# Kernel optimization log

Hardware: AMD Instinct MI355X
Metric: run time of the kernel (lower is better)

## Reference

```python
import jax, jax.numpy as jnp
import numpy as np

N_U = 20000; N_I = 20000; D = 256
NNZ = 600000; EGG = 300000; EDD = 300000; B = 8192
DROP = 0.1; LAM2 = 1e-7


def _attention(x, W, a, edges):
    # GAT-style attention over sampled relationship edges (src -> tgt).
    n, d = x.shape
    h = x @ W                                  # [n, d]
    src, tgt = edges[0], edges[1]
    e = jax.nn.leaky_relu((h @ a[:d])[src] + (h @ a[d:])[tgt], 0.2)  # [E]
    m = jax.ops.segment_max(e, tgt, num_segments=n)
    m = jnp.where(jnp.isfinite(m), m, 0.0)
    ex = jnp.exp(e - m[tgt])
    denom = jax.ops.segment_sum(ex, tgt, num_segments=n)             # [n]
    num = jax.ops.segment_sum(ex[:, None] * h[src], tgt, num_segments=n)  # [n, d]
    return num / (denom[:, None] + 1e-9)


def _spmm(rows, cols, vals, x, n_out):
    # sparse [n_out, n_in] @ dense [n_in, d]
    return jax.ops.segment_sum(vals[:, None] * x[cols], rows, num_segments=n_out)


def _mlp(x, W1, b1, W2, b2, W3, b3):
    h = jax.nn.relu(x @ W1 + b1)
    h = jax.nn.relu(h @ W2 + b2)
    return (h @ W3 + b3)[..., 0]


def setup_inputs() -> dict:
    key = jax.random.key(0)
    ks = jax.random.split(key, 24)
    s = 0.02
    inp = {
        'E_g_0': jax.random.normal(ks[0], (N_U, D), jnp.float32) * s,
        'E_d_0': jax.random.normal(ks[1], (N_I, D), jnp.float32) * s,
        'att_W': jax.random.normal(ks[2], (D, D), jnp.float32) * s,
        'att_a': jax.random.normal(ks[3], (2 * D,), jnp.float32) * s,
        'att1_W': jax.random.normal(ks[4], (D, D), jnp.float32) * s,
        'att1_a': jax.random.normal(ks[5], (2 * D,), jnp.float32) * s,
        'W1': jax.random.normal(ks[6], (2 * D, D), jnp.float32) * s,
        'b1': jnp.zeros((D,), jnp.float32),
        'W2': jax.random.normal(ks[7], (D, D), jnp.float32) * s,
        'b2': jnp.zeros((D,), jnp.float32),
        'W3': jax.random.normal(ks[8], (D, 1), jnp.float32) * s,
        'b3': jnp.zeros((1,), jnp.float32),
        'M1': jax.random.normal(ks[9], (2 * D, D), jnp.float32) * s,
        'mb1': jnp.zeros((D,), jnp.float32),
        'M2': jax.random.normal(ks[10], (D, D), jnp.float32) * s,
        'mb2': jnp.zeros((D,), jnp.float32),
        'adj_vals': jax.random.uniform(ks[11], (NNZ,), jnp.float32),
        'uids': jax.random.randint(ks[12], (B,), 0, N_U, jnp.int32),
        'iids': jax.random.randint(ks[13], (B,), 0, N_I, jnp.int32),
        'pos': jax.random.randint(ks[14], (B,), 0, N_I, jnp.int32),
        'neg': jax.random.randint(ks[15], (B,), 0, N_I, jnp.int32),
        'gene_edges': jax.random.randint(ks[16], (2, EGG), 0, N_U, jnp.int32),
        'drug_edges': jax.random.randint(ks[17], (2, EDD), 0, N_I, jnp.int32),
        'adj_rows': jax.random.randint(ks[18], (NNZ,), 0, N_U, jnp.int32),
        'adj_cols': jax.random.randint(ks[19], (NNZ,), 0, N_I, jnp.int32),
        'drop1': jax.random.bernoulli(ks[20], 1.0 - DROP, (NNZ,)),
        'drop2': jax.random.bernoulli(ks[21], 1.0 - DROP, (NNZ,)),
    }
    return inp


def reference(E_g_0, E_d_0, att_W, att_a, att1_W, att1_a, W1, b1, W2, b2, W3, b3,
              M1, mb1, M2, mb2, adj_vals, uids, iids, pos, neg,
              gene_edges, drug_edges, adj_rows, adj_cols, drop1, drop2):
    # Attention-modulated layer-0 embeddings
    E_d0 = 0.1 * _attention(E_d_0, att_W, att_a, drug_edges) + E_d_0
    E_g0 = 0.1 * _attention(E_g_0, att_W, att_a, gene_edges) + E_g_0

    # sparse_dropout + spmm (two independent dropout draws, as in the source)
    scale = 1.0 / (1.0 - DROP)
    v1 = adj_vals * drop1.astype(adj_vals.dtype) * scale
    v2 = adj_vals * drop2.astype(adj_vals.dtype) * scale
    E_g = _spmm(adj_rows, adj_cols, v1, E_d0, N_U)   # adj @ E_d0
    E_d = _spmm(adj_cols, adj_rows, v2, E_g0, N_I)   # adj.T @ E_g0

    u = E_g[uids]; p = E_d[pos]; ng = E_d[neg]
    pos_s = _mlp(jnp.concatenate([u, p], axis=-1), W1, b1, W2, b2, W3, b3)
    neg_s = _mlp(jnp.concatenate([u, ng], axis=-1), W1, b1, W2, b2, W3, b3)

    # BCE-with-logits (labels 1 for pos, 0 for neg) + BPR term
    loss_pos = jnp.mean(jax.nn.softplus(-pos_s))
    loss_neg = jnp.mean(jax.nn.softplus(neg_s))
    loss_bpr = jnp.mean(jax.nn.softplus(-(pos_s - neg_s)))
    loss_r = loss_pos + loss_neg + loss_bpr

    params = (E_g_0, E_d_0, att_W, att_a, att1_W, att1_a,
              W1, b1, W2, b2, W3, b3, M1, mb1, M2, mb2)
    loss_reg = LAM2 * sum(jnp.sum(p_ * p_) for p_ in params)

    loss = loss_reg + loss_r  # loss_s == 0
    return jnp.stack([loss, loss_r, jnp.zeros((), loss.dtype)])
```

## Files before the change

### kernel.cpp

```cpp
#include <hip/hip_runtime.h>
#include <math.h>

#define N_NODES 20000
#define D       256
#define NNZ     600000
#define NEDGE   300000
#define BATCH   8192
#define DROP_SCALE (1.0f/0.9f)
#define LAM2_F  1e-7f

#define M_PAD   20096
#define CSTRIDE 20032

#define C_ATT 56
#define C_ADJ 80

#define BINW 320
#define NBIN 63
#define TILE_E 2048
#define EPT 8
#define T_ATT ((NEDGE + TILE_E - 1) / TILE_E)
#define T_ADJ ((NNZ + TILE_E - 1) / TILE_E)
#define NBLK_P1 (2 * T_ATT + 2 * T_ADJ)
#define CAP_BIN_ATT 5376
#define CAP_BIN_ADJ 9216

#define FP8_SCALE 256.0f
#define VSCALE    58980.0f
#define INV_VSCALE (1.0f/58980.0f)

typedef unsigned short u16;
typedef unsigned char  u8;
typedef __attribute__((ext_vector_type(8))) short bf16x8;
typedef __attribute__((ext_vector_type(4))) float f32x4;
typedef __attribute__((ext_vector_type(2))) float f32x2;
typedef __attribute__((ext_vector_type(4))) unsigned v4u;

__device__ inline float wave_reduce(float v) {
    #pragma unroll
    for (int off = 32; off > 0; off >>= 1) v += __shfl_down(v, off, 64);
    return v;
}

__device__ inline float softplus_f(float x) {
    float r = log1pf(__expf(-fabsf(x)));
    return x > 0.f ? x + r : r;
}

__device__ inline u16 f2bf(float f) {
    unsigned u = __float_as_uint(f);
    unsigned r = u + 0x7fff + ((u >> 16) & 1);
    return (u16)(r >> 16);
}
__device__ inline float bf2f(u16 b) { return __uint_as_float(((unsigned)b) << 16); }

__device__ inline u16 f2h(float f) {
    _Float16 h = (_Float16)f;
    return __builtin_bit_cast(u16, h);
}
__device__ inline float h2f(u16 b) {
    return (float)__builtin_bit_cast(_Float16, b);
}

__device__ inline unsigned f32x4_to_fp8x4(float a, float b, float c, float d) {
    int r = 0;
    r = __builtin_amdgcn_cvt_pk_fp8_f32(a, b, r, false);
    r = __builtin_amdgcn_cvt_pk_fp8_f32(c, d, r, true);
    return (unsigned)r;
}
__device__ inline u8 f32_to_fp8(float a) {
    int r = __builtin_amdgcn_cvt_pk_fp8_f32(a, a, 0, false);
    return (u8)(r & 0xff);
}

__device__ inline void gld_lds16(const void* g, void* l) {
    __builtin_amdgcn_global_load_lds((const __attribute__((address_space(1))) void*)g,
                                     (__attribute__((address_space(3))) void*)l, 16, 0, 0);
}

struct RegArgs { const float* p[14]; int n[14]; };

__device__ inline void gemm_tile_k(const u16* __restrict__ A, const u16* __restrict__ BT, int K,
                                   int bm, int bn, short (*As)[32], short (*Bs)[32],
                                   f32x4 (&acr)[4][4]) {
    int tid = threadIdx.x, wave = tid >> 6, lane = tid & 63;
    int sr = lane >> 2, sc = (lane & 3) * 8;
    int wr = (wave >> 1) * 64, wc = (wave & 1) * 64;
    int fr = lane & 15, fk = (lane >> 4) * 8;
    for (int k0 = 0; k0 < K; k0 += 32) {
        #pragma unroll
        for (int j = 0; j < 2; j++) {
            int r0 = wave * 32 + j * 16;
            gld_lds16(A  + (size_t)(bm + r0 + sr) * K + k0 + sc, &As[r0][0]);
            gld_lds16(BT + (size_t)(bn + r0 + sr) * K + k0 + sc, &Bs[r0][0]);
        }
        __syncthreads();
        bf16x8 af[4], bfr[4];
        #pragma unroll
        for (int i = 0; i < 4; i++) af[i]  = *(const bf16x8*)&As[wr + i*16 + fr][fk];
        #pragma unroll
        for (int j = 0; j < 4; j++) bfr[j] = *(const bf16x8*)&Bs[wc + j*16 + fr][fk];
        #pragma unroll
        for (int i = 0; i < 4; i++)
            #pragma unroll
            for (int j = 0; j < 4; j++)
                acr[i][j] = __builtin_amdgcn_mfma_f32_16x16x32_bf16(af[i], bfr[j], acr[i][j], 0, 0, 0);
        __syncthreads();
    }
}

__global__ __launch_bounds__(1024) void init_kernel(const float* __restrict__ att_W,
                                                    const float* __restrict__ att_a,
                                                    float* __restrict__ wlv, float* __restrict__ wrv,
                                                    int* __restrict__ zbase, int zwords) {
    int tid = threadIdx.x;
    for (int i = tid; i < zwords; i += 1024) zbase[i] = 0;
    int t = tid & 255, q = tid >> 8;
    float s1 = 0.f, s2 = 0.f;
    for (int n = q * 64; n < q * 64 + 64; n++) {
        float w = att_W[(size_t)t * D + n];
        s1 += w * att_a[n];
        s2 += w * att_a[D + n];
    }
    __shared__ float r1[4][256], r2[4][256];
    r1[q][t] = s1; r2[q][t] = s2;
    __syncthreads();
    if (q == 0) {
        wlv[t] = r1[0][t] + r1[1][t] + r1[2][t] + r1[3][t];
        wrv[t] = r2[0][t] + r2[1][t] + r2[2][t] + r2[3][t];
    }
}

#define NB_CAST (2 * M_PAD / 4)
#define NB_T1   (D * D / 256)
#define NB_T2   (2 * D * D / 256)
#define NB_T3   (D * D / 256)
#define NB_PREP (NB_CAST + NB_T1 + NB_T2 + NB_T3)
#define NB_REG  448
__global__ __launch_bounds__(256) void p1prep_kernel(
        const int* __restrict__ dtgt, const int* __restrict__ dsrc,
        const int* __restrict__ gtgt, const int* __restrict__ gsrc,
        const int* __restrict__ ar,   const int* __restrict__ ac,
        const float* __restrict__ vals,
        const void* __restrict__ drop1, const void* __restrict__ drop2,
        int* __restrict__ pcur, unsigned* __restrict__ attbin, uint2* __restrict__ adjbin,
        const float* __restrict__ E_g, const float* __restrict__ E_d,
        u16* __restrict__ Eg_bf, u16* __restrict__ Ed_bf,
        const float* __restrict__ att_W,
        const float* __restrict__ W1, const float* __restrict__ W2,
        u16* __restrict__ attWT, u16* __restrict__ W1T, u16* __restrict__ W2T,
        const float* __restrict__ wlv, const float* __restrict__ wrv,
        float* __restrict__ hl_g, float* __restrict__ hr_g,
        float* __restrict__ hl_d, float* __restrict__ hr_d,
        float* __restrict__ regp, RegArgs ra, float* __restrict__ acc) {
    if (blockIdx.x < NBLK_P1) {
        __shared__ int hist[NBIN];
        __shared__ int basep[NBIN];
        for (int i = threadIdx.x; i < NBIN; i += 256) hist[i] = 0;
        __syncthreads();

        int b = blockIdx.x;
        int s, t0;
        if (b < T_ATT)               { s = 0; t0 = b; }
        else if (b < 2 * T_ATT)      { s = 1; t0 = b - T_ATT; }
        else if (b < 2*T_ATT + T_ADJ){ s = 2; t0 = b - 2 * T_ATT; }
        else                         { s = 3; t0 = b - 2 * T_ATT - T_ADJ; }
        int base = t0 * TILE_E;
        int regN = (s < 2) ? NEDGE : NNZ;

        int bins[EPT], rank[EPT];
        unsigned key[EPT], pay[EPT];
        float pv[EPT];

        if (s < 2) {
            const int* tgt = (s == 0) ? dtgt : gtgt;
            const int* src = (s == 0) ? dsrc : gsrc;
            #pragma unroll
            for (int e = 0; e < EPT; e++) {
                int idx = base + e * 256 + threadIdx.x;
                rank[e] = -1;
                if (idx < regN) {
                    int k = __builtin_nontemporal_load(tgt + idx);
                    int sv = __builtin_nontemporal_load(src + idx);
                    key[e] = (unsigned)k; pay[e] = (unsigned)sv;
                    bins[e] = k / BINW;
                    rank[e] = atomicAdd(&hist[bins[e]], 1);
                }
            }
        } else {
            const int* keyp = (s == 2) ? ar : ac;
            const int* othp = (s == 2) ? ac : ar;
            const void* drp = (s == 2) ? drop1 : drop2;
            bool nzs = ((const u8*)drp)[4 * threadIdx.x + 1] != 0;
            const bool bf = __popcll(__ballot(nzs)) > 16;
            #pragma unroll
            for (int e = 0; e < EPT; e++) {
                int idx = base + e * 256 + threadIdx.x;
                rank[e] = -1;
                if (idx < regN) {
                    bool keep = bf ? (__builtin_nontemporal_load((const u8*)drp + idx) != 0)
                                   : (__builtin_nontemporal_load((const unsigned*)drp + idx) != 0);
                    if (keep) {
                        int k = __builtin_nontemporal_load(keyp + idx);
                        float v = __builtin_nontemporal_load(vals + idx) * DROP_SCALE;
                        int oth = __builtin_nontemporal_load(othp + idx);
                        key[e] = (unsigned)k; pay[e] = (unsigned)oth; pv[e] = v;
                        bins[e] = k / BINW;
                        rank[e] = atomicAdd(&hist[bins[e]], 1);
                    }
                }
            }
        }
        __syncthreads();
        for (int i = threadIdx.x; i < NBIN; i += 256) {
            int h = hist[i];
            basep[i] = h ? atomicAdd(&pcur[s * NBIN + i], h) : 0;
        }
        __syncthreads();
        if (s < 2) {
            unsigned* seg = attbin + (size_t)s * NBIN * CAP_BIN_ATT;
            #pragma unroll
            for (int e = 0; e < EPT; e++) {
                if (rank[e] < 0) continue;
                int pos = basep[bins[e]] + rank[e];
                if (pos < CAP_BIN_ATT)
                    seg[(size_t)bins[e] * CAP_BIN_ATT + pos] = key[e] | (pay[e] << 16);
            }
        } else {
            uint2* seg = adjbin + (size_t)(s - 2) * NBIN * CAP_BIN_ADJ;
            #pragma unroll
            for (int e = 0; e < EPT; e++) {
                if (rank[e] < 0) continue;
                int pos = basep[bins[e]] + rank[e];
                if (pos < CAP_BIN_ADJ) {
                    uint2 pr; pr.x = key[e] | (pay[e] << 16); pr.y = __float_as_uint(pv[e]);
                    seg[(size_t)bins[e] * CAP_BIN_ADJ + pos] = pr;
                }
            }
        }
    } else {
        int bid = blockIdx.x - NBLK_P1;
        int w = threadIdx.x >> 6, lane = threadIdx.x & 63;
        if (bid < NB_CAST) {
            int wid  = (bid * 256 + threadIdx.x) >> 6;
            int is_d = (wid >= M_PAD);
            int row  = is_d ? wid - M_PAD : wid;
            u16* dst = (is_d ? Ed_bf : Eg_bf) + (size_t)row * D;
            float s3 = 0.f;
            if (row >= N_NODES) {
                ((ushort4*)dst)[lane] = make_ushort4(0, 0, 0, 0);
            } else {
                const float* src = (is_d ? E_d : E_g) + (size_t)row * D;
                float4 e  = ((const float4*)src)[lane];
                float4 l4 = ((const float4*)wlv)[lane];
                float4 r4 = ((const float4*)wrv)[lane];
                ((ushort4*)dst)[lane] = make_ushort4(f2bf(e.x), f2bf(e.y), f2bf(e.z), f2bf(e.w));
                float s1 = e.x*l4.x + e.y*l4.y + e.z*l4.z + e.w*l4.w;
                float s2 = e.x*r4.x + e.y*r4.y + e.z*r4.z + e.w*r4.w;
                s3 = e.x*e.x + e.y*e.y + e.z*e.z + e.w*e.w;
                s1 = wave_reduce(s1); s2 = wave_reduce(s2);
                if (lane == 0) {
                    if (is_d) { hl_d[row] = s1; hr_d[row] = s2; }
                    else      { hl_g[row] = s1; hr_g[row] = s2; }
                }
            }
            s3 = wave_reduce(s3);
            __shared__ float sm3[4];
            if (lane == 0) sm3[threadIdx.x >> 6] = s3;
            __syncthreads();
            if (threadIdx.x == 0) regp[bid] = sm3[0] + sm3[1] + sm3[2] + sm3[3];
        } else if (bid < NB_CAST + NB_T1) {
            int o = (bid - NB_CAST) * 256 + threadIdx.x;
            int n = o >> 8, k = o & 255;
            attWT[o] = f2bf(att_W[(size_t)k * D + n]);
        } else if (bid < NB_CAST + NB_T1 + NB_T2) {
            int o = (bid - NB_CAST - NB_T1) * 256 + threadIdx.x;
            int n = o / (2 * D), k = o - n * (2 * D);
            W1T[o] = f2bf(W1[(size_t)k * D + n]);
        } else if (bid < NB_PREP) {
            int o = (bid - NB_CAST - NB_T1 - NB_T2) * 256 + threadIdx.x;
            int n = o >> 8, k = o & 255;
            W2T[o] = f2bf(W2[(size_t)k * D + n]);
        } else {
            int rb = bid - NB_PREP;
            const float* p = ra.p[rb >> 5];
            int n = ra.n[rb >> 5];
            int base = (rb & 31) * 4096;
            if (base >= n) return;
            float sum = 0.f;
            if (base + 4096 <= n) {
                const float4* p4 = (const float4*)(p + base);
                float4 v = p4[threadIdx.x];
                sum += v.x*v.x + v.y*v.y + v.z*v.z + v.w*v.w;
                v = p4[256 + threadIdx.x];
                sum += v.x*v.x + v.y*v.y + v.z*v.z + v.w*v.w;
                v = p4[512 + threadIdx.x];
                sum += v.x*v.x + v.y*v.y + v.z*v.z + v.w*v.w;
                v = p4[768 + threadIdx.x];
                sum += v.x*v.x + v.y*v.y + v.z*v.z + v.w*v.w;
            } else {
                for (int i = base + threadIdx.x; i < n; i += 256) { float v = p[i]; sum += v * v; }
            }
            sum = wave_reduce(sum);
            __shared__ float smr[4];
            if (lane == 0) smr[w] = sum;
            __syncthreads();
            if (threadIdx.x == 0)
                atomicAdd(&acc[0], smr[0] + smr[1] + smr[2] + smr[3]);
        }
    }
}

#define NB_P2   (4 * NBIN)
#define NB_ATTG ((M_PAD / 128) * 4)
__global__ __launch_bounds__(256) void p2gemm_kernel(
        const int* __restrict__ pcur, const unsigned* __restrict__ attbin,
        const uint2* __restrict__ adjbin,
        const float* __restrict__ hl_d, const float* __restrict__ hr_d,
        const float* __restrict__ hl_g, const float* __restrict__ hr_g,
        int* __restrict__ cnt, unsigned* __restrict__ srcs, unsigned* __restrict__ adj,
        const u16* __restrict__ Eg_bf, const u16* __restrict__ Ed_bf,
        const u16* __restrict__ attWT, u8* __restrict__ h_g, u8* __restrict__ h_d) {
    if (blockIdx.x < NB_P2) {
        int s   = blockIdx.x / NBIN;
        int bin = blockIdx.x - s * NBIN;
        int nodeBase = bin * BINW;
        __shared__ int cur[BINW];
        for (int t = threadIdx.x; t < BINW; t += 256) cur[t] = 0;
        __syncthreads();
        if (s < 2) {
            int m = pcur[s * NBIN + bin]; if (m > CAP_BIN_ATT) m = CAP_BIN_ATT;
            const unsigned* seg = attbin + ((size_t)s * NBIN + bin) * CAP_BIN_ATT;
            const float* hl = (s == 0) ? hl_d : hl_g;
            const float* hr = (s == 0) ? hr_d : hr_g;
            for (int k = threadIdx.x; k < m; k += 256) {
                unsigned e = seg[k];
                int lk  = (int)(e & 0xFFFFu) - nodeBase;
                int src = (int)(e >> 16);
                float ev = hl[src] + hr[nodeBase + lk];
                ev = ev > 0.f ? ev : 0.2f * ev;
                u16 xh = f2h(__expf(ev));
                int c = atomicAdd(&cur[lk], 1);
                if (c < C_ATT)
                    srcs[(size_t)s * N_NODES * C_ATT + (size_t)(nodeBase + lk) * C_ATT + c] =
                        (unsigned)src | ((unsigned)xh << 16);
            }
            __syncthreads();
            for (int t = threadIdx.x; t < BINW; t += 256) {
                int node = nodeBase + t;
                if (node < N_NODES) {
                    int n = cur[t]; if (n > C_ATT) n = C_ATT;
                    cnt[s * CSTRIDE + node] = n;
                }
            }
        } else {
            int m = pcur[s * NBIN + bin]; if (m > CAP_BIN_ADJ) m = CAP_BIN_ADJ;
            const uint2* seg = adjbin + ((size_t)(s - 2) * NBIN + bin) * CAP_BIN_ADJ;
            for (int k = threadIdx.x; k < m; k += 256) {
                uint2 e = seg[k];
                int lk  = (int)(e.x & 0xFFFFu) - nodeBase;
                int oth = (int)(e.x >> 16);
                float v = __uint_as_float(e.y);
                unsigned pk = ((unsigned)(v * VSCALE + 0.5f) << 16) | (unsigned)oth;
                int c = atomicAdd(&cur[lk], 1);
                if (c < C_ADJ)
                    adj[(size_t)(s - 2) * N_NODES * C_ADJ + (size_t)(nodeBase + lk) * C_ADJ + c] = pk;
            }
            __syncthreads();
            for (int t = threadIdx.x; t < BINW; t += 256) {
                int node = nodeBase + t;
                if (node < N_NODES) {
                    int n = cur[t]; if (n > C_ADJ) n = C_ADJ;
                    cnt[s * CSTRIDE + node] = n;
                }
            }
        }
    } else {
        int t  = blockIdx.x - NB_P2;
        int z  = t / (2 * (M_PAD / 128));
        int r  = t - z * (2 * (M_PAD / 128));
        int by = r / (M_PAD / 128);
        int bx = r - by * (M_PAD / 128);
        const u16* A = z ? Ed_bf : Eg_bf;
        u8* C = z ? h_d : h_g;
        __shared__ __align__(16) short As[128][32];
        __shared__ __align__(16) short Bs[128][32];
        int wave = threadIdx.x >> 6, lane = threadIdx.x & 63;
        int bm = bx * 128, bn = by * 128;
        f32x4 acr[4][4];
        #pragma unroll
        for (int i = 0; i < 4; i++)
            #pragma unroll
            for (int j = 0; j < 4; j++)
                #pragma unroll
                for (int q = 0; q < 4; q++) acr[i][j][q] = 0.f;
        gemm_tile_k(A, attWT, D, bm, bn, As, Bs, acr);
        int wr = (wave >> 1) * 64, wc = (wave & 1) * 64, fr = lane & 15;
        #pragma unroll
        for (int j = 0; j < 4; j++) {
            int col = bn + wc + j * 16 + fr;
            #pragma unroll
            for (int i = 0; i < 4; i++) {
                #pragma unroll
                for (int q = 0; q < 4; q++) {
                    int row = bm + wr + i * 16 + (lane >> 4) * 4 + q;
                    if (row < N_NODES)
                        C[(size_t)row * D + col] = f32_to_fp8(acr[i][j][q] * FP8_SCALE);
                }
            }
        }
    }
}

__global__ __launch_bounds__(256) void gemm_bf16(const u16* __restrict__ A, const u16* __restrict__ BT,
                                                 void* __restrict__ C, int M, int N, int K,
                                                 const float* __restrict__ bias, int do_relu, int out_mode,
                                                 const float* __restrict__ w3) {
    __shared__ __align__(16) short As[128][32];
    __shared__ __align__(16) short Bs[128][32];
    int tid = threadIdx.x;
    int wave = tid >> 6, lane = tid & 63;
    int bm = blockIdx.x * 128, bn = blockIdx.y * 128;

    f32x4 acr[4][4];
    #pragma unroll
    for (int i = 0; i < 4; i++)
        #pragma unroll
        for (int j = 0; j < 4; j++)
            #pragma unroll
            for (int r = 0; r < 4; r++) acr[i][j][r] = 0.f;

    gemm_tile_k(A, BT, K, bm, bn, As, Bs, acr);

    int wr = (wave >> 1) * 64, wc = (wave & 1) * 64, fr = lane & 15;

    if (out_mode == 2) {
        __shared__ float sacc[128];
        for (int t = tid; t < 128; t += 256) sacc[t] = 0.f;
        __syncthreads();
        float bvj[4], w3j[4];
        #pragma unroll
        for (int j = 0; j < 4; j++) {
            int col = bn + wc + j * 16 + fr;
            bvj[j] = bias[col];
            w3j[j] = w3[col];
        }
        #pragma unroll
        for (int i = 0; i < 4; i++) {
            #pragma unroll
            for (int r = 0; r < 4; r++) {
                float rs = 0.f;
                #pragma unroll
                for (int j = 0; j < 4; j++) {
                    float v = fmaxf(acr[i][j][r] + bvj[j], 0.f);
                    rs += v * w3j[j];
                }
                rs += __shfl_xor(rs, 1, 64);
                rs += __shfl_xor(rs, 2, 64);
                rs += __shfl_xor(rs, 4, 64);
                rs += __shfl_xor(rs, 8, 64);
                if (fr == 0)
                    atomicAdd(&sacc[wr + i * 16 + (lane >> 4) * 4 + r], rs);
            }
        }
        __syncthreads();
        float* sb = (float*)C;
        for (int t = tid; t < 128; t += 256)
            atomicAdd(&sb[bm + t], sacc[t]);
        return;
    }

    #pragma unroll
    for (int j = 0; j < 4; j++) {
        int col = bn + wc + j * 16 + fr;
        float bv = bias ? bias[col] : 0.f;
        #pragma unroll
        for (int i = 0; i < 4; i++) {
            #pragma unroll
            for (int r = 0; r < 4; r++) {
                int row = bm + wr + i * 16 + (lane >> 4) * 4 + r;
                if (row < M) {
                    float v = acr[i][j][r] + bv;
                    if (do_relu) v = fmaxf(v, 0.f);
                    ((u16*)C)[(size_t)row * N + col] = f2bf(v);
                }
            }
        }
    }
}

__global__ __launch_bounds__(256) void att_kernel(const u8* __restrict__ h_d, const u8* __restrict__ h_g,
                                                  const int* __restrict__ cur, const unsigned* __restrict__ srcs,
                                                  const u16* __restrict__ Ed_bf, const u16* __restrict__ Eg_bf,
                                                  u8* __restrict__ E_d0p, u8* __restrict__ E_g0p) {
    int wid  = (blockIdx.x * blockDim.x + threadIdx.x) >> 6;
    int lane = threadIdx.x & 63;
    if (wid >= 2 * N_NODES) return;
    int is_g = (wid >= N_NODES);
    int node = is_g ? wid - N_NODES : wid;
    const unsigned* h32 = (const unsigned*)(is_g ? h_g : h_d);
    int reg = is_g ? 1 : 0;
    const unsigned* sv = srcs + (size_t)reg * N_NODES * C_ATT + (size_t)node * C_ATT;
    int n = cur[reg * CSTRIDE + node];
    if (n > C_ATT) n = C_ATT;
    float ax = 0.f, ay = 0.f, az = 0.f, aw = 0.f, denom = 0.f;
    int k = 0;
    for (; k + 8 <= n; k += 8) {
        v4u qa = __builtin_nontemporal_load((const v4u*)(sv + k));
        v4u qb = __builtin_nontemporal_load((const v4u*)(sv + k + 4));
        unsigned g[8]; float x[8];
        #pragma unroll
        for (int j = 0; j < 4; j++) {
            g[j]     = h32[((size_t)(qa[j] & 0xFFFFu) << 6) + lane];
            g[4 + j] = h32[((size_t)(qb[j] & 0xFFFFu) << 6) + lane];
            x[j]     = h2f((u16)(qa[j] >> 16));
            x[4 + j] = h2f((u16)(qb[j] >> 16));
        }
        #pragma unroll
        for (int j = 0; j < 8; j++) {
            denom += x[j];
            f32x2 lo = __builtin_amdgcn_cvt_pk_f32_fp8(g[j], false);
            f32x2 hi = __builtin_amdgcn_cvt_pk_f32_fp8(g[j], true);
            ax += x[j]*lo[0]; ay += x[j]*lo[1]; az += x[j]*hi[0]; aw += x[j]*hi[1];
        }
    }
    for (; k + 4 <= n; k += 4) {
        v4u qa = __builtin_nontemporal_load((const v4u*)(sv + k));
        unsigned g[4]; float x[4];
        #pragma unroll
        for (int j = 0; j < 4; j++) {
            g[j] = h32[((size_t)(qa[j] & 0xFFFFu) << 6) + lane];
            x[j] = h2f((u16)(qa[j] >> 16));
        }
        #pragma unroll
        for (int j = 0; j < 4; j++) {
            denom += x[j];
            f32x2 lo = __builtin_amdgcn_cvt_pk_f32_fp8(g[j], false);
            f32x2 hi = __builtin_amdgcn_cvt_pk_f32_fp8(g[j], true);
            ax += x[j]*lo[0]; ay += x[j]*lo[1]; az += x[j]*hi[0]; aw += x[j]*hi[1];
        }
    }
    for (; k < n; k++) {
        unsigned q = sv[k];
        float xv = h2f((u16)(q >> 16));
        unsigned g = h32[((size_t)(q & 0xFFFFu) << 6) + lane];
        denom += xv;
        f32x2 lo = __builtin_amdgcn_cvt_pk_f32_fp8(g, false);
        f32x2 hi = __builtin_amdgcn_cvt_pk_f32_fp8(g, true);
        ax += xv*lo[0]; ay += xv*lo[1]; az += xv*hi[0]; aw += xv*hi[1];
    }
    float sc = 0.1f / (denom + 1e-9f);
    const u16* E0b = is_g ? Eg_bf : Ed_bf;
    u8*       out  = is_g ? E_g0p : E_d0p;
    ushort4 b4 = ((const ushort4*)(E0b + (size_t)node * D))[lane];
    unsigned pk = f32x4_to_fp8x4(FP8_SCALE * bf2f(b4.x) + sc * ax, FP8_SCALE * bf2f(b4.y) + sc * ay,
                                 FP8_SCALE * bf2f(b4.z) + sc * az, FP8_SCALE * bf2f(b4.w) + sc * aw);
    ((unsigned*)(out + (size_t)node * D))[lane] = pk;
}

__global__ __launch_bounds__(256) void pull_kernel(const int* __restrict__ uids, const int* __restrict__ pos,
                                                   const int* __restrict__ neg,
                                                   const int* __restrict__ cur, const unsigned* __restrict__ adj,
                                                   const u8* __restrict__ E_d0p, const u8* __restrict__ E_g0p,
                                                   u16* __restrict__ X) {
    int wid  = (blockIdx.x * blockDim.x + threadIdx.x) >> 6;
    int lane = threadIdx.x & 63;
    if (wid >= 3 * BATCH) return;
    int type = wid >> 13;
    int b    = wid & (BATCH - 1);
    int node, reg; const u8* E;
    if (type == 0)      { node = uids[b]; reg = 2; E = E_d0p; }
    else if (type == 1) { node = pos[b];  reg = 3; E = E_g0p; }
    else                { node = neg[b];  reg = 3; E = E_g0p; }
    const unsigned* E32 = (const unsigned*)E;
    const unsigned* av = adj + (size_t)(reg - 2) * N_NODES * C_ADJ + (size_t)node * C_ADJ;
    int n = cur[reg * CSTRIDE + node];
    if (n > C_ADJ) n = C_ADJ;
    float ax = 0.f, ay = 0.f, az = 0.f, aw = 0.f;
    int k = 0;
    for (; k + 8 <= n; k += 8) {
        v4u qa = __builtin_nontemporal_load((const v4u*)(av + k));
        v4u qb = __builtin_nontemporal_load((const v4u*)(av + k + 4));
        unsigned g[8]; float v[8];
        #pragma unroll
        for (int j = 0; j < 4; j++) {
            g[j]     = E32[((size_t)(qa[j] & 0xFFFFu) << 6) + lane];
            g[4 + j] = E32[((size_t)(qb[j] & 0xFFFFu) << 6) + lane];
            v[j]     = (float)(qa[j] >> 16) * INV_VSCALE;
            v[4 + j] = (float)(qb[j] >> 16) * INV_VSCALE;
        }
        #pragma unroll
        for (int j = 0; j < 8; j++) {
            f32x2 lo = __builtin_amdgcn_cvt_pk_f32_fp8(g[j], false);
            f32x2 hi = __builtin_amdgcn_cvt_pk_f32_fp8(g[j], true);
            ax += v[j]*lo[0]; ay += v[j]*lo[1]; az += v[j]*hi[0]; aw += v[j]*hi[1];
        }
    }
    for (; k + 4 <= n; k += 4) {
        v4u qa = __builtin_nontemporal_load((const v4u*)(av + k));
        unsigned g[4]; float v[4];
        #pragma unroll
        for (int j = 0; j < 4; j++) {
            g[j] = E32[((size_t)(qa[j] & 0xFFFFu) << 6) + lane];
            v[j] = (float)(qa[j] >> 16) * INV_VSCALE;
        }
        #pragma unroll
        for (int j = 0; j < 4; j++) {
            f32x2 lo = __builtin_amdgcn_cvt_pk_f32_fp8(g[j], false);
            f32x2 hi = __builtin_amdgcn_cvt_pk_f32_fp8(g[j], true);
            ax += v[j]*lo[0]; ay += v[j]*lo[1]; az += v[j]*hi[0]; aw += v[j]*hi[1];
        }
    }
    for (; k < n; k++) {
        unsigned q = av[k];
        int c = q & 0xFFFF;
        float v = (float)(q >> 16) * INV_VSCALE;
        unsigned g = E32[((size_t)c << 6) + lane];
        f32x2 lo = __builtin_amdgcn_cvt_pk_f32_fp8(g, false);
        f32x2 hi = __builtin_amdgcn_cvt_pk_f32_fp8(g, true);
        ax += v*lo[0]; ay += v*lo[1]; az += v*hi[0]; aw += v*hi[1];
    }
    const float inv = 1.0f / FP8_SCALE;
    ushort4 r = make_ushort4(f2bf(ax * inv), f2bf(ay * inv), f2bf(az * inv), f2bf(aw * inv));
    if (type == 0) {
        ((ushort4*)(X + (size_t)b * 2 * D))[lane] = r;
        ((ushort4*)(X + (size_t)(BATCH + b) * 2 * D))[lane] = r;
    } else if (type == 1) {
        ((ushort4*)(X + (size_t)b * 2 * D + D))[lane] = r;
    } else {
        ((ushort4*)(X + (size_t)(BATCH + b) * 2 * D + D))[lane] = r;
    }
}

#define NB_TAIL 16
__global__ __launch_bounds__(256) void tail_kernel(const float* __restrict__ s,
                                                   const float* __restrict__ b3p,
                                                   const float* __restrict__ regp,
                                                   float* __restrict__ acc, float* __restrict__ out) {
    int bid = blockIdx.x, tid = threadIdx.x;
    int w = tid >> 6, lane = tid & 63;
    float b3 = b3p[0];
    float lp = 0.f, ln = 0.f, lb = 0.f, rsum = 0.f;
    for (int i = bid * 256 + tid; i < BATCH; i += NB_TAIL * 256) {
        float ps = s[i] + b3, ns = s[BATCH + i] + b3;
        lp += softplus_f(-ps);
        ln += softplus_f(ns);
        lb += softplus_f(-(ps - ns));
    }
    for (int i = bid * 256 + tid; i < NB_CAST; i += NB_TAIL * 256) rsum += regp[i];
    lp = wave_reduce(lp); ln = wave_reduce(ln); lb = wave_reduce(lb); rsum = wave_reduce(rsum);
    __shared__ float sm[4][4];
    if (lane == 0) { sm[0][w] = lp; sm[1][w] = ln; sm[2][w] = lb; sm[3][w] = rsum; }
    __syncthreads();
    if (tid == 0) {
        float a = 0.f, b = 0.f, c = 0.f, rg = 0.f;
        for (int i = 0; i < 4; i++) { a += sm[0][i]; b += sm[1][i]; c += sm[2][i]; rg += sm[3][i]; }
        atomicAdd(&acc[1], a); atomicAdd(&acc[2], b); atomicAdd(&acc[3], c);
        atomicAdd(&acc[0], rg);
    }
    __syncthreads();
    __shared__ int lastf;
    if (tid == 0) {
        __threadfence();
        unsigned t = atomicAdd((unsigned*)&acc[8], 1u);
        lastf = (t == NB_TAIL - 1);
    }
    __syncthreads();
    if (!lastf || tid != 0) return;
    float a0 = __hip_atomic_load(&acc[0], __ATOMIC_RELAXED, __HIP_MEMORY_SCOPE_AGENT);
    float a1 = __hip_atomic_load(&acc[1], __ATOMIC_RELAXED, __HIP_MEMORY_SCOPE_AGENT);
    float a2 = __hip_atomic_load(&acc[2], __ATOMIC_RELAXED, __HIP_MEMORY_SCOPE_AGENT);
    float a3 = __hip_atomic_load(&acc[3], __ATOMIC_RELAXED, __HIP_MEMORY_SCOPE_AGENT);
    float lr = (a1 + a2 + a3) * (1.0f / (float)BATCH);
    out[0] = LAM2_F * a0 + lr;
    out[1] = lr;
    out[2] = 0.f;
}

extern "C" void kernel_launch(void* const* d_in, const int* in_sizes, int n_in,
                              void* d_out, int out_size, void* d_ws, size_t ws_size,
                              hipStream_t stream) {
    (void)n_in; (void)out_size; (void)ws_size;
    const float* E_g_0   = (const float*)d_in[0];
    const float* E_d_0   = (const float*)d_in[1];
    const float* att_W   = (const float*)d_in[2];
    const float* att_a   = (const float*)d_in[3];
    const float* W1      = (const float*)d_in[6];
    const float* b1      = (const float*)d_in[7];
    const float* W2      = (const float*)d_in[8];
    const float* b2      = (const float*)d_in[9];
    const float* W3      = (const float*)d_in[10];
    const float* b3      = (const float*)d_in[11];
    const float* adj_vals= (const float*)d_in[16];
    const int*   uids    = (const int*)d_in[17];
    const int*   pos     = (const int*)d_in[19];
    const int*   neg     = (const int*)d_in[20];
    const int*   gene_e  = (const int*)d_in[21];
    const int*   drug_e  = (const int*)d_in[22];
    const int*   adj_rows= (const int*)d_in[23];
    const int*   adj_cols= (const int*)d_in[24];
    const void*  drop1   = d_in[25];
    const void*  drop2   = d_in[26];

    char* ws = (char*)d_ws;
    size_t cur_off = 0;
    auto take = [&](size_t bytes) -> void* {
        void* p = ws + cur_off;
        cur_off += (bytes + 255) & ~(size_t)255;
        return p;
    };
    u16* Eg_bf = (u16*)take((size_t)M_PAD * D * 2);
    u16* Ed_bf = (u16*)take((size_t)M_PAD * D * 2);
    u16* X     = Eg_bf;
    u16* attWT = (u16*)take((size_t)D * D * 2);
    u16* W1T   = (u16*)take((size_t)D * 2 * D * 2);
    u16* W2T   = (u16*)take((size_t)D * D * 2);
    u8*  h_g   = (u8*)take((size_t)M_PAD * D);
    u8*  h_d   = (u8*)take((size_t)M_PAD * D);
    u8*  E_g0p = (u8*)take((size_t)N_NODES * D);
    u8*  E_d0p = (u8*)take((size_t)N_NODES * D);
    u16* H1    = (u16*)take((size_t)2 * BATCH * D * 2);
    float* hl_g = (float*)take((size_t)N_NODES * 4);
    float* hr_g = (float*)take((size_t)N_NODES * 4);
    float* hl_d = (float*)take((size_t)N_NODES * 4);
    float* hr_d = (float*)take((size_t)N_NODES * 4);
    float* wlv  = (float*)take((size_t)D * 4);
    float* wrv  = (float*)take((size_t)D * 4);
    float* regp = (float*)take((size_t)NB_CAST * 4);
    unsigned* srcs = (unsigned*)take((size_t)2 * N_NODES * C_ATT * 4);
    unsigned* adj  = (unsigned*)take((size_t)2 * N_NODES * C_ADJ * 4);
    int*   cnt  = (int*)take((size_t)4 * CSTRIDE * 4);
    unsigned* attbin = (unsigned*)take((size_t)2 * NBIN * CAP_BIN_ATT * 4);
    uint2*    adjbin = (uint2*)take((size_t)2 * NBIN * CAP_BIN_ADJ * 8);
    int*      pcur = (int*)take((size_t)4 * NBIN * 4);
    float*    acc  = (float*)take(256);
    float*    sbuf = (float*)take((size_t)2 * BATCH * 4);
    int zwords = (int)((((char*)sbuf + (size_t)2 * BATCH * 4) - (char*)pcur) / 4);

    init_kernel<<<1, 1024, 0, stream>>>(att_W, att_a, wlv, wrv, pcur, zwords);

    RegArgs ra;
    for (int i = 0; i < 14; i++) { ra.p[i] = (const float*)d_in[i + 2]; ra.n[i] = in_sizes[i + 2]; }
    p1prep_kernel<<<NBLK_P1 + NB_PREP + NB_REG, 256, 0, stream>>>(
        drug_e + NEDGE, drug_e, gene_e + NEDGE, gene_e,
        adj_rows, adj_cols, adj_vals, drop1, drop2,
        pcur, attbin, adjbin,
        E_g_0, E_d_0, Eg_bf, Ed_bf, att_W, W1, W2,
        attWT, W1T, W2T, wlv, wrv, hl_g, hr_g, hl_d, hr_d, regp, ra, acc);

    p2gemm_kernel<<<NB_P2 + NB_ATTG, 256, 0, stream>>>(
        pcur, attbin, adjbin, hl_d, hr_d, hl_g, hr_g, cnt, srcs, adj,
        Eg_bf, Ed_bf, attWT, h_g, h_d);

    att_kernel<<<10000, 256, 0, stream>>>(h_d, h_g, cnt, srcs,
                                          Ed_bf, Eg_bf, E_d0p, E_g0p);

    pull_kernel<<<6144, 256, 0, stream>>>(uids, pos, neg, cnt, adj, E_d0p, E_g0p, X);

    gemm_bf16<<<dim3(2 * BATCH / 128, 2, 1), 256, 0, stream>>>(
        X, W1T, H1, 2 * BATCH, D, 2 * D, b1, 1, 0, nullptr);
    gemm_bf16<<<dim3(2 * BATCH / 128, 2, 1), 256, 0, stream>>>(
        H1, W2T, sbuf, 2 * BATCH, D, D, b2, 1, 2, W3);

    tail_kernel<<<NB_TAIL, 256, 0, stream>>>(sbuf, b3, regp, acc, (float*)d_out);
}
```

Before: 299.9 us.

## Filter adjacency edges to batch-needed rows via bitmaps; fuse W2 GEMM halves

The init kernel now builds bitmaps marking which user rows (uids) and item rows (pos/neg) the batch actually needs. The adjacency binning pass uses them to drop nonzeros whose output row is never read, so the later sparse aggregation only processes edges that matter. The per-bin capacity shrinks to match. The second MLP GEMM also loops over both column halves in one block and writes scores directly, which removes the y-dimension split, the atomics and zeroing of sbuf. The risk is that fewer blocks run for that GEMM, and bin capacity could overflow if many batch rows concentrate in one bin.

Result: slower. 313.8 us (+4.6%).

```diff
diff --git a/kernel.cpp b/kernel.cpp
--- a/kernel.cpp
+++ b/kernel.cpp
@@ -23,7 +23,7 @@
 #define T_ADJ ((NNZ + TILE_E - 1) / TILE_E)
 #define NBLK_P1 (2 * T_ATT + 2 * T_ADJ)
 #define CAP_BIN_ATT 5376
-#define CAP_BIN_ADJ 9216
+#define CAP_BIN_ADJ 6144
 
 #define FP8_SCALE 256.0f
 #define VSCALE    58980.0f
@@ -111,10 +111,23 @@
 
 __global__ __launch_bounds__(1024) void init_kernel(const float* __restrict__ att_W,
                                                     const float* __restrict__ att_a,
+                                                    const int* __restrict__ uids,
+                                                    const int* __restrict__ pos,
+                                                    const int* __restrict__ neg,
                                                     float* __restrict__ wlv, float* __restrict__ wrv,
+                                                    unsigned* __restrict__ bm2, unsigned* __restrict__ bm3,
                                                     int* __restrict__ zbase, int zwords) {
+    __shared__ unsigned lb2[640], lb3[640];
+    __shared__ float r1[4][256], r2[4][256];
     int tid = threadIdx.x;
     for (int i = tid; i < zwords; i += 1024) zbase[i] = 0;
+    for (int i = tid; i < 640; i += 1024) { lb2[i] = 0; lb3[i] = 0; }
+    __syncthreads();
+    for (int i = tid; i < BATCH; i += 1024) {
+        int v = uids[i]; atomicOr(&lb2[v >> 5], 1u << (v & 31));
+        int p = pos[i];  atomicOr(&lb3[p >> 5], 1u << (p & 31));
+        int g = neg[i];  atomicOr(&lb3[g >> 5], 1u << (g & 31));
+    }
     int t = tid & 255, q = tid >> 8;
     float s1 = 0.f, s2 = 0.f;
     for (int n = q * 64; n < q * 64 + 64; n++) {
@@ -122,13 +135,13 @@
         s1 += w * att_a[n];
         s2 += w * att_a[D + n];
     }
-    __shared__ float r1[4][256], r2[4][256];
     r1[q][t] = s1; r2[q][t] = s2;
     __syncthreads();
     if (q == 0) {
         wlv[t] = r1[0][t] + r1[1][t] + r1[2][t] + r1[3][t];
         wrv[t] = r2[0][t] + r2[1][t] + r2[2][t] + r2[3][t];
     }
+    for (int i = tid; i < 640; i += 1024) { bm2[i] = lb2[i]; bm3[i] = lb3[i]; }
 }
 
 #define NB_CAST (2 * M_PAD / 4)
@@ -143,6 +156,7 @@
         const int* __restrict__ ar,   const int* __restrict__ ac,
         const float* __restrict__ vals,
         const void* __restrict__ drop1, const void* __restrict__ drop2,
+        const unsigned* __restrict__ bm2, const unsigned* __restrict__ bm3,
         int* __restrict__ pcur, unsigned* __restrict__ attbin, uint2* __restrict__ adjbin,
         const float* __restrict__ E_g, const float* __restrict__ E_d,
         u16* __restrict__ Eg_bf, u16* __restrict__ Ed_bf,
@@ -191,6 +205,7 @@
             const int* keyp = (s == 2) ? ar : ac;
             const int* othp = (s == 2) ? ac : ar;
             const void* drp = (s == 2) ? drop1 : drop2;
+            const unsigned* bm = (s == 2) ? bm2 : bm3;
             bool nzs = ((const u8*)drp)[4 * threadIdx.x + 1] != 0;
             const bool bf = __popcll(__ballot(nzs)) > 16;
             #pragma unroll
@@ -198,15 +213,17 @@
                 int idx = base + e * 256 + threadIdx.x;
                 rank[e] = -1;
                 if (idx < regN) {
-                    bool keep = bf ? (__builtin_nontemporal_load((const u8*)drp + idx) != 0)
-                                   : (__builtin_nontemporal_load((const unsigned*)drp + idx) != 0);
-                    if (keep) {
-                        int k = __builtin_nontemporal_load(keyp + idx);
-                        float v = __builtin_nontemporal_load(vals + idx) * DROP_SCALE;
-                        int oth = __builtin_nontemporal_load(othp + idx);
-                        key[e] = (unsigned)k; pay[e] = (unsigned)oth; pv[e] = v;
-                        bins[e] = k / BINW;
-                        rank[e] = atomicAdd(&hist[bins[e]], 1);
+                    int k = __builtin_nontemporal_load(keyp + idx);
+                    if ((bm[k >> 5] >> (k & 31)) & 1) {
+                        bool keep = bf ? (__builtin_nontemporal_load((const u8*)drp + idx) != 0)
+                                       : (__builtin_nontemporal_load((const unsigned*)drp + idx) != 0);
+                        if (keep) {
+                            float v = __builtin_nontemporal_load(vals + idx) * DROP_SCALE;
+                            int oth = __builtin_nontemporal_load(othp + idx);
+                            key[e] = (unsigned)k; pay[e] = (unsigned)oth; pv[e] = v;
+                            bins[e] = k / BINW;
+                            rank[e] = atomicAdd(&hist[bins[e]], 1);
+                        }
                     }
                 }
             }
@@ -420,8 +437,56 @@
     __shared__ __align__(16) short Bs[128][32];
     int tid = threadIdx.x;
     int wave = tid >> 6, lane = tid & 63;
-    int bm = blockIdx.x * 128, bn = blockIdx.y * 128;
-
+    int bm = blockIdx.x * 128;
+    int wr = (wave >> 1) * 64, wc = (wave & 1) * 64, fr = lane & 15;
+
+    if (out_mode == 2) {
+        __shared__ float sacc[128];
+        for (int t = tid; t < 128; t += 256) sacc[t] = 0.f;
+        #pragma unroll
+        for (int half = 0; half < 2; half++) {
+            int bnh = half * 128;
+            f32x4 acr[4][4];
+            #pragma unroll
+            for (int i = 0; i < 4; i++)
+                #pragma unroll
+                for (int j = 0; j < 4; j++)
+                    #pragma unroll
+                    for (int r = 0; r < 4; r++) acr[i][j][r] = 0.f;
+            gemm_tile_k(A, BT, K, bm, bnh, As, Bs, acr);
+            float bvj[4], w3j[4];
+            #pragma unroll
+            for (int j = 0; j < 4; j++) {
+                int col = bnh + wc + j * 16 + fr;
+                bvj[j] = bias[col];
+                w3j[j] = w3[col];
+            }
+            #pragma unroll
+            for (int i = 0; i < 4; i++) {
+                #pragma unroll
+                for (int r = 0; r < 4; r++) {
+                    float rs = 0.f;
+                    #pragma unroll
+                    for (int j = 0; j < 4; j++) {
+                        float v = fmaxf(acr[i][j][r] + bvj[j], 0.f);
+                        rs += v * w3j[j];
+                    }
+                    rs += __shfl_xor(rs, 1, 64);
+                    rs += __shfl_xor(rs, 2, 64);
+                    rs += __shfl_xor(rs, 4, 64);
+                    rs += __shfl_xor(rs, 8, 64);
+                    if (fr == 0)
+                        atomicAdd(&sacc[wr + i * 16 + (lane >> 4) * 4 + r], rs);
+                }
+            }
+        }
+        __syncthreads();
+        float* sb = (float*)C;
+        for (int t = tid; t < 128; t += 256) sb[bm + t] = sacc[t];
+        return;
+    }
+
+    int bn = blockIdx.y * 128;
     f32x4 acr[4][4];
     #pragma unroll
     for (int i = 0; i < 4; i++)
@@ -431,44 +496,6 @@
             for (int r = 0; r < 4; r++) acr[i][j][r] = 0.f;
 
     gemm_tile_k(A, BT, K, bm, bn, As, Bs, acr);
-
-    int wr = (wave >> 1) * 64, wc = (wave & 1) * 64, fr = lane & 15;
-
-    if (out_mode == 2) {
-        __shared__ float sacc[128];
-        for (int t = tid; t < 128; t += 256) sacc[t] = 0.f;
-        __syncthreads();
-        float bvj[4], w3j[4];
-        #pragma unroll
-        for (int j = 0; j < 4; j++) {
-            int col = bn + wc + j * 16 + fr;
-            bvj[j] = bias[col];
-            w3j[j] = w3[col];
-        }
-        #pragma unroll
-        for (int i = 0; i < 4; i++) {
-            #pragma unroll
-            for (int r = 0; r < 4; r++) {
-                float rs = 0.f;
-                #pragma unroll
-                for (int j = 0; j < 4; j++) {
-                    float v = fmaxf(acr[i][j][r] + bvj[j], 0.f);
-                    rs += v * w3j[j];
-                }
-                rs += __shfl_xor(rs, 1, 64);
-                rs += __shfl_xor(rs, 2, 64);
-                rs += __shfl_xor(rs, 4, 64);
-                rs += __shfl_xor(rs, 8, 64);
-                if (fr == 0)
-                    atomicAdd(&sacc[wr + i * 16 + (lane >> 4) * 4 + r], rs);
-            }
-        }
-        __syncthreads();
-        float* sb = (float*)C;
-        for (int t = tid; t < 128; t += 256)
-            atomicAdd(&sb[bm + t], sacc[t]);
-        return;
-    }
 
     #pragma unroll
     for (int j = 0; j < 4; j++) {
@@ -727,6 +754,9 @@
     float* wlv  = (float*)take((size_t)D * 4);
     float* wrv  = (float*)take((size_t)D * 4);
     float* regp = (float*)take((size_t)NB_CAST * 4);
+    float* sbuf = (float*)take((size_t)2 * BATCH * 4);
+    unsigned* bm2 = (unsigned*)take(4096);
+    unsigned* bm3 = (unsigned*)take(4096);
     unsigned* srcs = (unsigned*)take((size_t)2 * N_NODES * C_ATT * 4);
     unsigned* adj  = (unsigned*)take((size_t)2 * N_NODES * C_ADJ * 4);
     int*   cnt  = (int*)take((size_t)4 * CSTRIDE * 4);
@@ -734,16 +764,16 @@
     uint2*    adjbin = (uint2*)take((size_t)2 * NBIN * CAP_BIN_ADJ * 8);
     int*      pcur = (int*)take((size_t)4 * NBIN * 4);
     float*    acc  = (float*)take(256);
-    float*    sbuf = (float*)take((size_t)2 * BATCH * 4);
-    int zwords = (int)((((char*)sbuf + (size_t)2 * BATCH * 4) - (char*)pcur) / 4);
-
-    init_kernel<<<1, 1024, 0, stream>>>(att_W, att_a, wlv, wrv, pcur, zwords);
+    int zwords = (int)((((char*)acc + 256) - (char*)pcur) / 4);
+
+    init_kernel<<<1, 1024, 0, stream>>>(att_W, att_a, uids, pos, neg,
+                                        wlv, wrv, bm2, bm3, pcur, zwords);
 
     RegArgs ra;
     for (int i = 0; i < 14; i++) { ra.p[i] = (const float*)d_in[i + 2]; ra.n[i] = in_sizes[i + 2]; }
     p1prep_kernel<<<NBLK_P1 + NB_PREP + NB_REG, 256, 0, stream>>>(
         drug_e + NEDGE, drug_e, gene_e + NEDGE, gene_e,
-        adj_rows, adj_cols, adj_vals, drop1, drop2,
+        adj_rows, adj_cols, adj_vals, drop1, drop2, bm2, bm3,
         pcur, attbin, adjbin,
         E_g_0, E_d_0, Eg_bf, Ed_bf, att_W, W1, W2,
         attWT, W1T, W2T, wlv, wrv, hl_g, hr_g, hl_d, hr_d, regp, ra, acc);
@@ -759,7 +789,7 @@
 
     gemm_bf16<<<dim3(2 * BATCH / 128, 2, 1), 256, 0, stream>>>(
         X, W1T, H1, 2 * BATCH, D, 2 * D, b1, 1, 0, nullptr);
-    gemm_bf16<<<dim3(2 * BATCH / 128, 2, 1), 256, 0, stream>>>(
+    gemm_bf16<<<dim3(2 * BATCH / 128, 1, 1), 256, 0, stream>>>(
         H1, W2T, sbuf, 2 * BATCH, D, D, b2, 1, 2, W3);
 
     tail_kernel<<<NB_TAIL, 256, 0, stream>>>(sbuf, b3, regp, acc, (float*)d_out);
```
